# Optimization experiments

Hardware: AMD Instinct MI355X
Metric: run time of the kernel (lower is better)

Reference implementation:

```python
import jax, jax.numpy as jnp
import numpy as np

B, LAT, H, K = 8, 128, 1024, 294
N, E = 100000, 1600000
XSIZE = 128.0
TAU = 0.5
STEPS = 3


def setup_inputs() -> dict:
    key = jax.random.key(0)
    ks = jax.random.split(key, 20)
    s_in = 1.0 / np.sqrt(LAT)
    s_h = 1.0 / np.sqrt(H)
    inp = {
        "latent": jax.random.normal(ks[0], (B, LAT), jnp.float32),
        "W0": jax.random.normal(ks[1], (LAT, H), jnp.float32) * s_in,
        "b0": jnp.zeros((H,), jnp.float32),
        "W1": jax.random.normal(ks[2], (H, H), jnp.float32) * s_h,
        "b1": jnp.zeros((H,), jnp.float32),
        "W2": jax.random.normal(ks[3], (H, H), jnp.float32) * s_h,
        "b2": jnp.zeros((H,), jnp.float32),
        "W3": jax.random.normal(ks[4], (H, H), jnp.float32) * s_h,
        "b3": jnp.zeros((H,), jnp.float32),
        # coefficient heads use normal(1e-4) init in the source
        "Wx": jax.random.normal(ks[5], (H, K), jnp.float32) * 1e-4,
        "bx": jnp.zeros((K,), jnp.float32),
        "Wy": jax.random.normal(ks[6], (H, K), jnp.float32) * 1e-4,
        "by": jnp.zeros((K,), jnp.float32),
        "Wz": jax.random.normal(ks[7], (H, K), jnp.float32) * 1e-4,
        "bz": jnp.zeros((K,), jnp.float32),
        # precomputed Zernike/spherical basis evaluated at the N coords: [K, N]
        "Z": jax.random.normal(ks[8], (K, N), jnp.float32),
        "edge_weights": jax.random.uniform(ks[9], (E,), jnp.float32),
        "edge_index": jax.random.randint(ks[10], (2, E), 0, N, jnp.int64),
    }
    return inp


def _decode_coefficients(latent, W0, b0, W1, b1, W2, b2, W3, b3,
                         Wx, bx, Wy, by, Wz, bz):
    h = jax.nn.relu(latent @ W0 + b0)
    for W, b in ((W1, b1), (W2, b2), (W3, b3)):
        h = jax.nn.relu(h + h @ W + b)  # residual MLP block
    return h @ Wx + bx, h @ Wy + by, h @ Wz + bz  # [B, K] each


def _diffuse(flow, edge_index, edge_weights):
    """Graph diffusion smoothing of per-node vectors. flow: [B, N, 3]."""
    src, dst = edge_index[0], edge_index[1]
    deg = jax.ops.segment_sum(edge_weights, dst, num_segments=N)
    deg = jnp.maximum(deg, 1e-6)[:, None, None]  # [N,1,1]
    f = jnp.transpose(flow, (1, 0, 2))  # [N, B, 3]
    w = edge_weights[:, None, None]
    for _ in range(STEPS):
        msg = f[src] * w                                        # gather  [E,B,3]
        agg = jax.ops.segment_sum(msg, dst, num_segments=N)     # scatter [N,B,3]
        f = (1.0 - TAU) * f + TAU * agg / deg
    return jnp.transpose(f, (1, 0, 2))  # [B, N, 3]


def reference(latent, W0, b0, W1, b1, W2, b2, W3, b3,
              Wx, bx, Wy, by, Wz, bz, Z, edge_weights, edge_index):
    cx, cy, cz = _decode_coefficients(latent, W0, b0, W1, b1, W2, b2, W3, b3,
                                      Wx, bx, Wy, by, Wz, bz)
    # basis evaluation: per-axis coefficients contracted with Zernike basis
    dx = jnp.einsum("bk,kn->bn", cx, Z)
    dy = jnp.einsum("bk,kn->bn", cy, Z)
    dz = jnp.einsum("bk,kn->bn", cz, Z)
    flow = (0.5 * XSIZE) * jnp.stack([dx, dy, dz], axis=-1)  # [B, N, 3]
    flow = _diffuse(flow, edge_index, edge_weights)
    reg = 1e-4 * jnp.sqrt(jnp.sum(cx ** 2 + cy ** 2 + cz ** 2))
    return flow, reg
```

## Files before the change

kernel.cpp:

```cpp
#include <hip/hip_runtime.h>
#include <math.h>

#define BB 8
#define LAT 128
#define HH 1024
#define KK 294
#define NN 100000
#define EE 1600000
#define NSTEPS 3
#define XS_HALF 64.0f

#define NB 391
#define CS 8
#define COB 28
#define COB2 30
#define EPT 8
#define EST 200000
#define EBLK 782
#define GON 40

#define F3NB 391
#define KPAD 320

__constant__ float ccoefT[KPAD * 24];


__device__ __forceinline__ void mlp_part_body(int bid, const float* __restrict__ hin,
                                              const float* __restrict__ W,
                                              float* __restrict__ part, int jdim) {
    int it = bid & 15;
    int bs = bid >> 4;
    int tx = threadIdx.x;
    int il = tx & 63;
    int jg = tx >> 6;
    int i = it * 64 + il;
    int j0 = bs * 64;

    __shared__ float hs[8 * 64];
    for (int u = tx; u < 512; u += 256) {
        int b = u >> 6, lj = u & 63;
        hs[u] = hin[b * jdim + j0 + lj];
    }
    __syncthreads();

    float acc[8];
#pragma unroll
    for (int b = 0; b < 8; ++b) acc[b] = 0.0f;
#pragma unroll
    for (int jj = 0; jj < 16; ++jj) {
        int lj = jg * 16 + jj;
        float w = W[(size_t)(j0 + lj) * HH + i];
#pragma unroll
        for (int b = 0; b < 8; ++b) acc[b] += hs[b * 64 + lj] * w;
    }

    __shared__ float red[4][8][64];
#pragma unroll
    for (int b = 0; b < 8; ++b) red[jg][b][il] = acc[b];
    __syncthreads();
    for (int u = tx; u < 512; u += 256) {
        int b = u >> 6, ii = u & 63;
        float s = red[0][b][ii] + red[1][b][ii] + red[2][b][ii] + red[3][b][ii];
        part[(size_t)bs * 8192 + b * HH + it * 64 + ii] = s;
    }
}

__device__ __forceinline__ void mlp_comb_body(int bid, const float* __restrict__ part,
                                              int nsplit, const float* __restrict__ resid,
                                              const float* __restrict__ bias,
                                              float* __restrict__ hout) {
    int idx = bid * 256 + threadIdx.x;
    if (idx >= BB * HH) return;
    int i = idx & (HH - 1);
    float s = bias[i];
    if (resid) s += resid[idx];
    for (int bs = 0; bs < nsplit; ++bs) s += part[(size_t)bs * 8192 + idx];
    hout[idx] = fmaxf(s, 0.0f);
}

__device__ __forceinline__ void count_body(int bid, const int* __restrict__ ei,
                                           int* __restrict__ cnt, int* __restrict__ rank) {
    int gid = bid * 256 + threadIdx.x;
    if (gid >= EST) return;
    int d[EPT];
#pragma unroll
    for (int j = 0; j < EPT; ++j) d[j] = ei[EE + gid + j * EST];
#pragma unroll
    for (int j = 0; j < EPT; ++j) {
        int p = atomicAdd(&cnt[d[j] * 4], 1);
        rank[gid + j * EST] = p;
    }
}

__device__ __forceinline__ void bsum_body(int bid, const int* __restrict__ cnt,
                                          int* __restrict__ bsum) {
    __shared__ int red[256];
    int i = bid * 256 + threadIdx.x;
    red[threadIdx.x] = (i < NN) ? cnt[i * 4] : 0;
    __syncthreads();
    for (int off = 128; off > 0; off >>= 1) {
        if ((int)threadIdx.x < off) red[threadIdx.x] += red[threadIdx.x + off];
        __syncthreads();
    }
    if (threadIdx.x == 0) bsum[bid] = red[0];
}

__device__ __forceinline__ void bscan_body(const int* __restrict__ bsum,
                                           int* __restrict__ bpre,
                                           int* __restrict__ offs) {
    __shared__ int A[512], Bf[512];
    int t = threadIdx.x;
    A[t] = (t < NB) ? bsum[t] : 0;
    A[t + 256] = (t + 256 < NB) ? bsum[t + 256] : 0;
    __syncthreads();
    int* s = A;
    int* d = Bf;
    for (int off = 1; off < 512; off <<= 1) {
        d[t] = s[t] + ((t >= off) ? s[t - off] : 0);
        int u = t + 256;
        d[u] = s[u] + ((u >= off) ? s[u - off] : 0);
        __syncthreads();
        int* tmp = s; s = d; d = tmp;
    }
    if (t < NB) bpre[t] = (t == 0) ? 0 : s[t - 1];
    int u = t + 256;
    if (u < NB) bpre[u] = s[u - 1];
    if (t == 0) offs[NN] = s[NB - 1];
}

__device__ __forceinline__ void offs_body(int bid, const int* __restrict__ cnt,
                                          const int* __restrict__ bpre,
                                          int* __restrict__ offs) {
    __shared__ int part[256];
    int t = threadIdx.x;
    int i = bid * 256 + t;
    int v = (i < NN) ? cnt[i * 4] : 0;
    part[t] = v;
    __syncthreads();
    for (int off = 1; off < 256; off <<= 1) {
        int u = (t >= off) ? part[t - off] : 0;
        __syncthreads();
        part[t] += u;
        __syncthreads();
    }
    if (i < NN) offs[i] = bpre[bid] + part[t] - v;
}

__device__ __forceinline__ void fill_body(int bid, const int* __restrict__ ei,
                                          const float* __restrict__ ew,
                                          const int* __restrict__ offs,
                                          const int* __restrict__ rank,
                                          int2* __restrict__ csr) {
    int gid = bid * 256 + threadIdx.x;
    if (gid >= EST) return;
    int s[EPT], d[EPT], r[EPT];
    float w[EPT];
#pragma unroll
    for (int j = 0; j < EPT; ++j) {
        int e = gid + j * EST;
        s[j] = ei[e];
        d[j] = ei[EE + e];
        w[j] = ew[e];
        r[j] = rank[e];
    }
#pragma unroll
    for (int j = 0; j < EPT; ++j) {
        int p = offs[d[j]] + r[j];
        int2 v;
        v.x = s[j];
        v.y = __float_as_int(w[j]);
        csr[p] = v;
    }
}

__device__ __forceinline__ void degcsr_body(int bid, const int* __restrict__ offs,
                                            const int2* __restrict__ csr,
                                            float* __restrict__ invh) {
    int n = bid * 256 + threadIdx.x;
    if (n >= NN) return;
    int beg = offs[n], end = offs[n + 1];
    float s = 0.0f;
    for (int i = beg; i < end; ++i) s += __int_as_float(csr[i].y);
    invh[n] = 0.5f / fmaxf(s, 1e-6f);
}

__device__ __forceinline__ void flow3_body(int bid, const float* __restrict__ Z,
                                           float* __restrict__ fout) {
    __shared__ float zl[4][4][8][64];

    int t = threadIdx.x;
    int lane = t & 63;
    int wu = __builtin_amdgcn_readfirstlane(t >> 6);

    int n = bid * 256 + (wu << 6) + lane;
    int nn = (n < NN) ? n : (NN - 1);
    const float* zn = Z + nn;

    float acc[24];
#pragma unroll
    for (int j = 0; j < 24; ++j) acc[j] = 0.0f;

    auto issue = [&](int cp) {
        int b = cp & 3;
#pragma unroll
        for (int d = 0; d < 8; ++d) {
            int r = cp * 8 + d;
            int rz = (r < KK) ? r : (KK - 1);
            __builtin_amdgcn_global_load_lds(
                (__attribute__((address_space(1))) unsigned int*)(zn + (size_t)rz * NN),
                (__attribute__((address_space(3))) unsigned int*)(&zl[wu][b][d][0]),
                4, 0, 0);
        }
    };

    issue(0); issue(1); issue(2);

#pragma unroll 1
    for (int c = 0; c < 37; ++c) {
        issue(c + 3);
        asm volatile("s_waitcnt vmcnt(24)" ::: "memory");
        __builtin_amdgcn_sched_barrier(0);
        int b = c & 3;
#pragma unroll
        for (int d = 0; d < 8; ++d) {
            float z = zl[wu][b][d][lane];
            const float* cf = &ccoefT[(c * 8 + d) * 24];
#pragma unroll
            for (int j = 0; j < 24; ++j) acc[j] = fmaf(cf[j], z, acc[j]);
        }
    }

    if (n < NN) {
        float buf4[24];
#pragma unroll
        for (int j = 0; j < 24; ++j) buf4[j] = XS_HALF * acc[j];
        float4* fr = (float4*)(fout + (size_t)n * 24);
#pragma unroll
        for (int q = 0; q < 6; ++q) fr[q] = ((const float4*)buf4)[q];
    }
}

__device__ __forceinline__ void reg_body(const float* __restrict__ coef,
                                         float* __restrict__ out_reg) {
    __shared__ float red[256];
    float s = 0.0f;
    for (int i = threadIdx.x; i < 3 * BB * KK; i += 256) {
        float v = coef[i];
        s += v * v;
    }
    red[threadIdx.x] = s;
    __syncthreads();
    for (int off = 128; off > 0; off >>= 1) {
        if ((int)threadIdx.x < off) red[threadIdx.x] += red[threadIdx.x + off];
        __syncthreads();
    }
    if (threadIdx.x == 0) out_reg[0] = 1e-4f * sqrtf(red[0]);
}


__global__ void K1_mlp0_count(const float* __restrict__ latent, const float* __restrict__ W0,
                              float* __restrict__ part, const int* __restrict__ ei,
                              int* __restrict__ cnt, int* __restrict__ rank) {
    if (blockIdx.x < 32) mlp_part_body(blockIdx.x, latent, W0, part, LAT);
    else count_body(blockIdx.x - 32, ei, cnt, rank);
}

__global__ void K2_comb0_bsum(const float* __restrict__ part, const float* __restrict__ b0,
                              float* __restrict__ hout, const int* __restrict__ cnt,
                              int* __restrict__ bsum) {
    if (blockIdx.x < 32) mlp_comb_body(blockIdx.x, part, 2, nullptr, b0, hout);
    else bsum_body(blockIdx.x - 32, cnt, bsum);
}

__global__ void K3_bscan_mlp1(const int* __restrict__ bsum, int* __restrict__ bpre,
                              int* __restrict__ offs, const float* __restrict__ hin,
                              const float* __restrict__ W1, float* __restrict__ part) {
    if (blockIdx.x == 0) bscan_body(bsum, bpre, offs);
    else mlp_part_body(blockIdx.x - 1, hin, W1, part, HH);
}

__global__ void K4_comb1_offs(const float* __restrict__ part, const float* __restrict__ resid,
                              const float* __restrict__ b1, float* __restrict__ hout,
                              const int* __restrict__ cnt, const int* __restrict__ bpre,
                              int* __restrict__ offs) {
    if (blockIdx.x < 32) mlp_comb_body(blockIdx.x, part, 16, resid, b1, hout);
    else offs_body(blockIdx.x - 32, cnt, bpre, offs);
}

__global__ void K5_mlp2_fill(const float* __restrict__ hin, const float* __restrict__ W2,
                             float* __restrict__ part, const int* __restrict__ ei,
                             const float* __restrict__ ew, const int* __restrict__ offs,
                             const int* __restrict__ rank, int2* __restrict__ csr) {
    if (blockIdx.x < 256) mlp_part_body(blockIdx.x, hin, W2, part, HH);
    else fill_body(blockIdx.x - 256, ei, ew, offs, rank, csr);
}

__global__ void K6_comb2_deg(const float* __restrict__ part, const float* __restrict__ resid,
                             const float* __restrict__ bias, float* __restrict__ hout,
                             const int* __restrict__ offs, const int2* __restrict__ csr,
                             float* __restrict__ invh) {
    if (blockIdx.x < 32) mlp_comb_body(blockIdx.x, part, 16, resid, bias, hout);
    else degcsr_body(blockIdx.x - 32, offs, csr, invh);
}

__global__ void K_mlp_part3(const float* __restrict__ hin, const float* __restrict__ W,
                            float* __restrict__ part) {
    mlp_part_body(blockIdx.x, hin, W, part, HH);
}

__global__ void K_mlp_comb(const float* __restrict__ part, const float* __restrict__ resid,
                           const float* __restrict__ bias, float* __restrict__ hout) {
    mlp_comb_body(blockIdx.x, part, 16, resid, bias, hout);
}

__global__ void k_coef_part(const float* __restrict__ h,
                            const float* __restrict__ Wx,
                            const float* __restrict__ Wy,
                            const float* __restrict__ Wz,
                            float* __restrict__ cpart) {
    int s = blockIdx.x / COB;
    int blk = blockIdx.x % COB;
    int o = blk * 256 + threadIdx.x;
    if (o >= 3 * BB * KK) return;
    int t = o / (BB * KK);
    int r = o % (BB * KK);
    int b = r / KK, k = r % KK;
    const float* W = (t == 0) ? Wx : ((t == 1) ? Wy : Wz);
    const float* hr = h + b * HH;
    int j0 = s * 128;
    float acc = 0.0f;
#pragma unroll 8
    for (int j = 0; j < 128; ++j) acc += hr[j0 + j] * W[(size_t)(j0 + j) * KK + k];
    cpart[(size_t)s * 7056 + o] = acc;
}

__global__ void k_coef_comb(const float* __restrict__ cpart,
                            const float* __restrict__ bx,
                            const float* __restrict__ by,
                            const float* __restrict__ bz,
                            float* __restrict__ coefT) {
    int o = blockIdx.x * 256 + threadIdx.x;
    if (o >= KPAD * 24) return;
    if (o >= 3 * BB * KK) {
        coefT[o] = 0.0f;
        return;
    }
    int t = o / (BB * KK);
    int r = o % (BB * KK);
    int b = r / KK;
    int k = r % KK;
    float s = ((t == 0) ? bx : ((t == 1) ? by : bz))[k];
#pragma unroll
    for (int i = 0; i < CS; ++i) s += cpart[(size_t)i * 7056 + o];
    coefT[k * 24 + b * 3 + t] = s;
}

__global__ void K11_flow_reg(const float* __restrict__ coefT, const float* __restrict__ Z,
                             float* __restrict__ fout, float* __restrict__ out_reg) {
    if (blockIdx.x < F3NB) flow3_body(blockIdx.x, Z, fout);
    else reg_body(coefT, out_reg);
}

__global__ void k_gather(const int* __restrict__ offs, const int2* __restrict__ csr,
                         const float* __restrict__ invh,
                         const float* __restrict__ fin, float* __restrict__ fout) {
    int idx = blockIdx.x * 256 + threadIdx.x;
    if (idx >= NN * 6) return;
    int n = idx / 6;
    int q = idx - n * 6;
    int beg = offs[n], end = offs[n + 1];
    const float4* f4 = (const float4*)fin;
    float4 acc = make_float4(0.f, 0.f, 0.f, 0.f);
    if (beg < end) {
        int2 e = csr[beg];
        for (int i = beg; i < end; ++i) {
            int2 en = (i + 1 < end) ? csr[i + 1] : e;
            float w = __int_as_float(e.y);
            float4 fv = f4[(size_t)e.x * 6 + q];
            acc.x += w * fv.x;
            acc.y += w * fv.y;
            acc.z += w * fv.z;
            acc.w += w * fv.w;
            e = en;
        }
    }
    float inv = invh[n];
    float4 fo = f4[(size_t)n * 6 + q];
    float4 r;
    r.x = 0.5f * fo.x + inv * acc.x;
    r.y = 0.5f * fo.y + inv * acc.y;
    r.z = 0.5f * fo.z + inv * acc.z;
    r.w = 0.5f * fo.w + inv * acc.w;
    ((float4*)fout)[(size_t)n * 6 + q] = r;
}

__global__ void k_gather_out(const int* __restrict__ offs, const int2* __restrict__ csr,
                             const float* __restrict__ invh,
                             const float* __restrict__ fin, float* __restrict__ out) {
    __shared__ float ls[GON * 24];
    int t = threadIdx.x;
    int n0 = blockIdx.x * GON;
    if (t < GON * 6) {
        int ln = t / 6, q = t - 6 * ln;
        int n = n0 + ln;
        if (n < NN) {
            int beg = offs[n], end = offs[n + 1];
            const float4* f4 = (const float4*)fin;
            float4 acc = make_float4(0.f, 0.f, 0.f, 0.f);
            if (beg < end) {
                int2 e = csr[beg];
                for (int i = beg; i < end; ++i) {
                    int2 en = (i + 1 < end) ? csr[i + 1] : e;
                    float w = __int_as_float(e.y);
                    float4 fv = f4[(size_t)e.x * 6 + q];
                    acc.x += w * fv.x;
                    acc.y += w * fv.y;
                    acc.z += w * fv.z;
                    acc.w += w * fv.w;
                    e = en;
                }
            }
            float inv = invh[n];
            float4 fo = f4[(size_t)n * 6 + q];
            float* d = &ls[ln * 24 + q * 4];
            d[0] = 0.5f * fo.x + inv * acc.x;
            d[1] = 0.5f * fo.y + inv * acc.y;
            d[2] = 0.5f * fo.z + inv * acc.z;
            d[3] = 0.5f * fo.w + inv * acc.w;
        }
    }
    __syncthreads();
    int cnt = NN - n0; if (cnt > GON) cnt = GON;
    int per_b = cnt * 3;
    for (int b = 0; b < BB; ++b) {
        for (int u = t; u < per_b; u += 256) {
            int n = u / 3;
            int c = u - 3 * n;
            out[(size_t)b * (NN * 3) + (size_t)n0 * 3 + u] = ls[n * 24 + b * 3 + c];
        }
    }
}

extern "C" void kernel_launch(void* const* d_in, const int* in_sizes, int n_in,
                              void* d_out, int out_size, void* d_ws, size_t ws_size,
                              hipStream_t stream) {
    const float* latent = (const float*)d_in[0];
    const float* W0 = (const float*)d_in[1];
    const float* b0 = (const float*)d_in[2];
    const float* W1 = (const float*)d_in[3];
    const float* b1 = (const float*)d_in[4];
    const float* W2 = (const float*)d_in[5];
    const float* b2 = (const float*)d_in[6];
    const float* W3 = (const float*)d_in[7];
    const float* b3 = (const float*)d_in[8];
    const float* Wx = (const float*)d_in[9];
    const float* bx = (const float*)d_in[10];
    const float* Wy = (const float*)d_in[11];
    const float* by = (const float*)d_in[12];
    const float* Wz = (const float*)d_in[13];
    const float* bz = (const float*)d_in[14];
    const float* Z  = (const float*)d_in[15];
    const float* ew = (const float*)d_in[16];
    const int*   ei = (const int*)d_in[17];
    float* out = (float*)d_out;

    float* p = (float*)d_ws;
    float* h_a     = p; p += 8192;
    float* h_b     = p; p += 8192;
    float* hp      = p; p += 16 * 8192;
    float* coef    = p; p += KPAD * 24;
    float* cpart   = p; p += CS * 7056;
    float* invh    = p; p += 100000;
    int*   cnt     = (int*)p; p += 400000;
    int*   offs    = (int*)p; p += 100016;
    int*   bsum    = (int*)p; p += 512;
    int*   bpre    = (int*)p; p += 512;
    int*   rank    = (int*)p; p += 1600000;
    int2*  csr     = (int2*)p; p += 2 * 1600000;
    float* fpart   = p; p += (size_t)2 * NN * 24;

    hipMemsetAsync(cnt, 0, 400000 * sizeof(int), stream);

    K1_mlp0_count<<<32 + EBLK, 256, 0, stream>>>(latent, W0, hp, ei, cnt, rank);
    K2_comb0_bsum<<<32 + NB, 256, 0, stream>>>(hp, b0, h_a, cnt, bsum);
    K3_bscan_mlp1<<<1 + 256, 256, 0, stream>>>(bsum, bpre, offs, h_a, W1, hp);
    K4_comb1_offs<<<32 + NB, 256, 0, stream>>>(hp, h_a, b1, h_b, cnt, bpre, offs);
    K5_mlp2_fill<<<256 + EBLK, 256, 0, stream>>>(h_b, W2, hp, ei, ew, offs, rank, csr);
    K6_comb2_deg<<<32 + NB, 256, 0, stream>>>(hp, h_b, b2, h_a, offs, csr, invh);
    K_mlp_part3<<<256, 256, 0, stream>>>(h_a, W3, hp);
    K_mlp_comb<<<32, 256, 0, stream>>>(hp, h_a, b3, h_b);
    k_coef_part<<<COB * CS, 256, 0, stream>>>(h_b, Wx, Wy, Wz, cpart);
    k_coef_comb<<<COB2, 256, 0, stream>>>(cpart, bx, by, bz, coef);
    hipMemcpyToSymbolAsync(HIP_SYMBOL(ccoefT), coef, KPAD * 24 * sizeof(float), 0,
                           hipMemcpyDeviceToDevice, stream);
    K11_flow_reg<<<F3NB + 1, 256, 0, stream>>>(coef, Z, fpart, out + (size_t)BB * NN * 3);

    float* f0 = fpart;
    float* f1 = fpart + (size_t)NN * 24;
    k_gather<<<(NN * 6 + 255) / 256, 256, 0, stream>>>(offs, csr, invh, f0, f1);
    k_gather<<<(NN * 6 + 255) / 256, 256, 0, stream>>>(offs, csr, invh, f1, f0);
    k_gather_out<<<(NN + GON - 1) / GON, 256, 0, stream>>>(offs, csr, invh, f0, out);
}
```

Measured before the change: 536.5 us.

## Fuse degree computation into gather kernels, unroll edge loop, compact counters

Removes the separate degree pass that read the CSR weights per node. Each gather thread now accumulates the weight sum alongside the messages and computes the inverse degree itself. The edge loop is unrolled by four so several CSR entries and feature gathers are in flight at once. The per-node counters go from a stride of four ints to dense storage, which shrinks the memset but puts more atomics contending within each cache line. Degree is recomputed redundantly in each of the three gathers and by all six quad threads per node.

```diff
diff --git a/kernel.cpp b/kernel.cpp
--- a/kernel.cpp
+++ b/kernel.cpp
@@ -87,7 +87,7 @@
     for (int j = 0; j < EPT; ++j) d[j] = ei[EE + gid + j * EST];
 #pragma unroll
     for (int j = 0; j < EPT; ++j) {
-        int p = atomicAdd(&cnt[d[j] * 4], 1);
+        int p = atomicAdd(&cnt[d[j]], 1);
         rank[gid + j * EST] = p;
     }
 }
@@ -96,7 +96,7 @@
                                           int* __restrict__ bsum) {
     __shared__ int red[256];
     int i = bid * 256 + threadIdx.x;
-    red[threadIdx.x] = (i < NN) ? cnt[i * 4] : 0;
+    red[threadIdx.x] = (i < NN) ? cnt[i] : 0;
     __syncthreads();
     for (int off = 128; off > 0; off >>= 1) {
         if ((int)threadIdx.x < off) red[threadIdx.x] += red[threadIdx.x + off];
@@ -134,7 +134,7 @@
     __shared__ int part[256];
     int t = threadIdx.x;
     int i = bid * 256 + t;
-    int v = (i < NN) ? cnt[i * 4] : 0;
+    int v = (i < NN) ? cnt[i] : 0;
     part[t] = v;
     __syncthreads();
     for (int off = 1; off < 256; off <<= 1) {
@@ -173,17 +173,6 @@
     }
 }
 
-__device__ __forceinline__ void degcsr_body(int bid, const int* __restrict__ offs,
-                                            const int2* __restrict__ csr,
-                                            float* __restrict__ invh) {
-    int n = bid * 256 + threadIdx.x;
-    if (n >= NN) return;
-    int beg = offs[n], end = offs[n + 1];
-    float s = 0.0f;
-    for (int i = beg; i < end; ++i) s += __int_as_float(csr[i].y);
-    invh[n] = 0.5f / fmaxf(s, 1e-6f);
-}
-
 __device__ __forceinline__ void flow3_body(int bid, const float* __restrict__ Z,
                                            float* __restrict__ fout) {
     __shared__ float zl[4][4][8][64];
@@ -295,12 +284,9 @@
     else fill_body(blockIdx.x - 256, ei, ew, offs, rank, csr);
 }
 
-__global__ void K6_comb2_deg(const float* __restrict__ part, const float* __restrict__ resid,
-                             const float* __restrict__ bias, float* __restrict__ hout,
-                             const int* __restrict__ offs, const int2* __restrict__ csr,
-                             float* __restrict__ invh) {
-    if (blockIdx.x < 32) mlp_comb_body(blockIdx.x, part, 16, resid, bias, hout);
-    else degcsr_body(blockIdx.x - 32, offs, csr, invh);
+__global__ void K6_comb2(const float* __restrict__ part, const float* __restrict__ resid,
+                         const float* __restrict__ bias, float* __restrict__ hout) {
+    mlp_comb_body(blockIdx.x, part, 16, resid, bias, hout);
 }
 
 __global__ void K_mlp_part3(const float* __restrict__ hin, const float* __restrict__ W,
@@ -362,7 +348,6 @@
 }
 
 __global__ void k_gather(const int* __restrict__ offs, const int2* __restrict__ csr,
-                         const float* __restrict__ invh,
                          const float* __restrict__ fin, float* __restrict__ fout) {
     int idx = blockIdx.x * 256 + threadIdx.x;
     if (idx >= NN * 6) return;
@@ -371,20 +356,36 @@
     int beg = offs[n], end = offs[n + 1];
     const float4* f4 = (const float4*)fin;
     float4 acc = make_float4(0.f, 0.f, 0.f, 0.f);
-    if (beg < end) {
-        int2 e = csr[beg];
-        for (int i = beg; i < end; ++i) {
-            int2 en = (i + 1 < end) ? csr[i + 1] : e;
-            float w = __int_as_float(e.y);
-            float4 fv = f4[(size_t)e.x * 6 + q];
-            acc.x += w * fv.x;
-            acc.y += w * fv.y;
-            acc.z += w * fv.z;
-            acc.w += w * fv.w;
-            e = en;
+    float wsum = 0.0f;
+    int i = beg;
+    for (; i + 4 <= end; i += 4) {
+        int2 e[4];
+#pragma unroll
+        for (int u = 0; u < 4; ++u) e[u] = csr[i + u];
+        float4 v[4];
+#pragma unroll
+        for (int u = 0; u < 4; ++u) v[u] = f4[(size_t)e[u].x * 6 + q];
+#pragma unroll
+        for (int u = 0; u < 4; ++u) {
+            float w = __int_as_float(e[u].y);
+            wsum += w;
+            acc.x += w * v[u].x;
+            acc.y += w * v[u].y;
+            acc.z += w * v[u].z;
+            acc.w += w * v[u].w;
         }
     }
-    float inv = invh[n];
+    for (; i < end; ++i) {
+        int2 e = csr[i];
+        float w = __int_as_float(e.y);
+        float4 fv = f4[(size_t)e.x * 6 + q];
+        wsum += w;
+        acc.x += w * fv.x;
+        acc.y += w * fv.y;
+        acc.z += w * fv.z;
+        acc.w += w * fv.w;
+    }
+    float inv = 0.5f / fmaxf(wsum, 1e-6f);
     float4 fo = f4[(size_t)n * 6 + q];
     float4 r;
     r.x = 0.5f * fo.x + inv * acc.x;
@@ -395,7 +396,6 @@
 }
 
 __global__ void k_gather_out(const int* __restrict__ offs, const int2* __restrict__ csr,
-                             const float* __restrict__ invh,
                              const float* __restrict__ fin, float* __restrict__ out) {
     __shared__ float ls[GON * 24];
     int t = threadIdx.x;
@@ -407,20 +407,36 @@
             int beg = offs[n], end = offs[n + 1];
             const float4* f4 = (const float4*)fin;
             float4 acc = make_float4(0.f, 0.f, 0.f, 0.f);
-            if (beg < end) {
-                int2 e = csr[beg];
-                for (int i = beg; i < end; ++i) {
-                    int2 en = (i + 1 < end) ? csr[i + 1] : e;
-                    float w = __int_as_float(e.y);
-                    float4 fv = f4[(size_t)e.x * 6 + q];
-                    acc.x += w * fv.x;
-                    acc.y += w * fv.y;
-                    acc.z += w * fv.z;
-                    acc.w += w * fv.w;
-                    e = en;
+            float wsum = 0.0f;
+            int i = beg;
+            for (; i + 4 <= end; i += 4) {
+                int2 e[4];
+#pragma unroll
+                for (int u = 0; u < 4; ++u) e[u] = csr[i + u];
+                float4 v[4];
+#pragma unroll
+                for (int u = 0; u < 4; ++u) v[u] = f4[(size_t)e[u].x * 6 + q];
+#pragma unroll
+                for (int u = 0; u < 4; ++u) {
+                    float w = __int_as_float(e[u].y);
+                    wsum += w;
+                    acc.x += w * v[u].x;
+                    acc.y += w * v[u].y;
+                    acc.z += w * v[u].z;
+                    acc.w += w * v[u].w;
                 }
             }
-            float inv = invh[n];
+            for (; i < end; ++i) {
+                int2 e = csr[i];
+                float w = __int_as_float(e.y);
+                float4 fv = f4[(size_t)e.x * 6 + q];
+                wsum += w;
+                acc.x += w * fv.x;
+                acc.y += w * fv.y;
+                acc.z += w * fv.z;
+                acc.w += w * fv.w;
+            }
+            float inv = 0.5f / fmaxf(wsum, 1e-6f);
             float4 fo = f4[(size_t)n * 6 + q];
             float* d = &ls[ln * 24 + q * 4];
             d[0] = 0.5f * fo.x + inv * acc.x;
@@ -470,8 +486,7 @@
     float* hp      = p; p += 16 * 8192;
     float* coef    = p; p += KPAD * 24;
     float* cpart   = p; p += CS * 7056;
-    float* invh    = p; p += 100000;
-    int*   cnt     = (int*)p; p += 400000;
+    int*   cnt     = (int*)p; p += 100000;
     int*   offs    = (int*)p; p += 100016;
     int*   bsum    = (int*)p; p += 512;
     int*   bpre    = (int*)p; p += 512;
@@ -479,14 +494,14 @@
     int2*  csr     = (int2*)p; p += 2 * 1600000;
     float* fpart   = p; p += (size_t)2 * NN * 24;
 
-    hipMemsetAsync(cnt, 0, 400000 * sizeof(int), stream);
+    hipMemsetAsync(cnt, 0, NN * sizeof(int), stream);
 
     K1_mlp0_count<<<32 + EBLK, 256, 0, stream>>>(latent, W0, hp, ei, cnt, rank);
     K2_comb0_bsum<<<32 + NB, 256, 0, stream>>>(hp, b0, h_a, cnt, bsum);
     K3_bscan_mlp1<<<1 + 256, 256, 0, stream>>>(bsum, bpre, offs, h_a, W1, hp);
     K4_comb1_offs<<<32 + NB, 256, 0, stream>>>(hp, h_a, b1, h_b, cnt, bpre, offs);
     K5_mlp2_fill<<<256 + EBLK, 256, 0, stream>>>(h_b, W2, hp, ei, ew, offs, rank, csr);
-    K6_comb2_deg<<<32 + NB, 256, 0, stream>>>(hp, h_b, b2, h_a, offs, csr, invh);
+    K6_comb2<<<32, 256, 0, stream>>>(hp, h_b, b2, h_a);
     K_mlp_part3<<<256, 256, 0, stream>>>(h_a, W3, hp);
     K_mlp_comb<<<32, 256, 0, stream>>>(hp, h_a, b3, h_b);
     k_coef_part<<<COB * CS, 256, 0, stream>>>(h_b, Wx, Wy, Wz, cpart);
@@ -497,7 +512,7 @@
 
     float* f0 = fpart;
     float* f1 = fpart + (size_t)NN * 24;
-    k_gather<<<(NN * 6 + 255) / 256, 256, 0, stream>>>(offs, csr, invh, f0, f1);
-    k_gather<<<(NN * 6 + 255) / 256, 256, 0, stream>>>(offs, csr, invh, f1, f0);
-    k_gather_out<<<(NN + GON - 1) / GON, 256, 0, stream>>>(offs, csr, invh, f0, out);
-}
+    k_gather<<<(NN * 6 + 255) / 256, 256, 0, stream>>>(offs, csr, f0, f1);
+    k_gather<<<(NN * 6 + 255) / 256, 256, 0, stream>>>(offs, csr, f1, f0);
+    k_gather_out<<<(NN + GON - 1) / GON, 256, 0, stream>>>(offs, csr, f0, out);
+}
```

Result: faster. 502.4 us (-6.4%).
